# Kernel optimization log

Measured on AMD Instinct MI355X. Metric: run time of the kernel, lower is better.

## Reference

```python
import jax, jax.numpy as jnp
import numpy as np

N, L, H, K, T = 768, 8, 64, 4, 3

def _mlp2(x, w1, b1, w2, b2):
    # Linear -> ReLU -> Linear -> ReLU (matches nn.Sequential in q/k/v MLPs)
    return jax.nn.relu(jax.nn.relu(x @ w1 + b1) @ w2 + b2)

def setup_inputs() -> dict:
    key = jax.random.key(0)
    ks = jax.random.split(key, 20)
    s = 1.0 / np.sqrt(H)
    def lin(k, din, dout):
        return jax.random.uniform(k, (din, dout), jnp.float32, -s, s)
    def bias(k, dout):
        return jax.random.uniform(k, (dout,), jnp.float32, -s, s)
    inp = {
        "h": jax.random.normal(ks[0], (N, L, H), jnp.float32),
        "coord": jax.random.normal(ks[1], (N, L, K, T), jnp.float32),
        "wq1": lin(ks[2], H, H), "bq1": bias(ks[3], H),
        "wq2": lin(ks[4], H, H), "bq2": bias(ks[5], H),
        "wk1": lin(ks[6], H, H), "bk1": bias(ks[7], H),
        "wk2": lin(ks[8], H, H), "bk2": bias(ks[9], H),
        "wv1": lin(ks[10], H, H), "bv1": bias(ks[11], H),
        "wv2": lin(ks[12], H, H), "bv2": bias(ks[13], H),
        "wc1": lin(ks[14], H, H), "bc1": bias(ks[15], H),
        # final coord layer: Linear(H, 4, bias=False), xavier gain=0.001
        "wc2": jax.random.normal(ks[16], (H, K), jnp.float32) * 0.001,
    }
    return inp

def reference(h, coord, wq1, bq1, wq2, bq2, wk1, bk1, wk2, bk2,
              wv1, bv1, wv2, bv2, wc1, bc1, wc2):
    q = _mlp2(h, wq1, bq1, wq2, bq2)          # [N, L, H]
    k = _mlp2(h, wk1, bk1, wk2, bk2)          # [N, L, H]
    v = _mlp2(h, wv1, bv1, wv2, bv2)          # [N, L, H]
    # scores[i, j, l] = <q_i, k_j> per frame l; softmax over neighbor axis j (dim=1)
    scores = jnp.einsum('ilh,jlh->ijl', q, k)
    alpha = jax.nn.softmax(scores, axis=1)     # [N, N, L]
    h_agg = jnp.einsum('ijl,jlh->ilh', alpha, v)
    cmv = jax.nn.relu(v @ wc1 + bc1) @ wc2     # coord_mlp(v): [N, L, 4]
    coord_diff = coord[:, None] - coord[None]  # [N, N, L, 4, 3]
    x_agg = jnp.einsum('ijlkt,ijl,jlk->ilkt', coord_diff, alpha, cmv)
    return (h + h_agg, coord + x_agg)
```

## Files before the change

kernel.cpp:

```cpp
#include <hip/hip_runtime.h>
#include <hip/hip_bf16.h>

#define NN 768
#define LL 8
#define HH 64
#define IT 16
#define SCP 772
#define ABP 776
#define XST 80

typedef __attribute__((ext_vector_type(8))) short bf16x8;
typedef __attribute__((ext_vector_type(4))) float f32x4;

__device__ __forceinline__ short f2bf(float x) {
    union { __hip_bfloat16 h; short s; } u;
    u.h = __float2bfloat16(x);
    return u.s;
}

__device__ __forceinline__ bf16x8 pack8(float4 lo, float4 hi) {
    bf16x8 r;
    r[0] = f2bf(lo.x); r[1] = f2bf(lo.y); r[2] = f2bf(lo.z); r[3] = f2bf(lo.w);
    r[4] = f2bf(hi.x); r[5] = f2bf(hi.y); r[6] = f2bf(hi.z); r[7] = f2bf(hi.w);
    return r;
}

__global__ __launch_bounds__(256) void prep_kernel(
    const float* __restrict__ wq1, const float* __restrict__ wq2,
    const float* __restrict__ wk1, const float* __restrict__ wk2,
    const float* __restrict__ wv1, const float* __restrict__ wv2,
    const float* __restrict__ wc1, const float* __restrict__ wc2,
    short* __restrict__ WT)
{
    const int idx = blockIdx.x * 256 + threadIdx.x;
    if (idx < 28672) {
        const int mm = idx >> 12, rem = idx & 4095;
        const int n = rem >> 6, kk = rem & 63;
        const float* srcs[7] = {wq1, wq2, wk1, wk2, wv1, wv2, wc1};
        WT[idx] = f2bf(srcs[mm][kk * 64 + n]);
    } else if (idx < 29696) {
        const int rem = idx - 28672;
        const int n = rem >> 6, kk = rem & 63;
        WT[idx] = (n < 4) ? f2bf(wc2[kk * 4 + n]) : (short)0;
    }
}

__device__ __forceinline__ void layer_mfma(bf16x8 a0, bf16x8 a1,
                                           const short* __restrict__ WT,
                                           const float* __restrict__ bias,
                                           int m, int quad, bool do_relu,
                                           f32x4 dout[4])
{
    #pragma unroll
    for (int nt = 0; nt < 4; ++nt) {
        const short* wp = WT + (nt * 16 + m) * 64 + quad * 8;
        bf16x8 b0 = *(const bf16x8*)wp;
        bf16x8 b1 = *(const bf16x8*)(wp + 32);
        f32x4 d = {0.f, 0.f, 0.f, 0.f};
        d = __builtin_amdgcn_mfma_f32_16x16x32_bf16(a0, b0, d, 0, 0, 0);
        d = __builtin_amdgcn_mfma_f32_16x16x32_bf16(a1, b1, d, 0, 0, 0);
        if (bias) {
            const float bb = bias[nt * 16 + m];
            #pragma unroll
            for (int rg = 0; rg < 4; ++rg) d[rg] += bb;
        }
        if (do_relu) {
            #pragma unroll
            for (int rg = 0; rg < 4; ++rg) d[rg] = fmaxf(d[rg], 0.f);
        }
        dout[nt] = d;
    }
}

__device__ __forceinline__ void d_to_X(const f32x4 d[4], short (*X)[XST],
                                       int m, int quad) {
    #pragma unroll
    for (int nt = 0; nt < 4; ++nt)
        #pragma unroll
        for (int rg = 0; rg < 4; ++rg)
            X[quad * 4 + rg][nt * 16 + m] = f2bf(d[nt][rg]);
}

__global__ __launch_bounds__(256) void qkv_kernel(
    const float* __restrict__ h, const float* __restrict__ coord,
    const float* __restrict__ bq1, const float* __restrict__ bq2,
    const float* __restrict__ bk1, const float* __restrict__ bk2,
    const float* __restrict__ bv1, const float* __restrict__ bv2,
    const float* __restrict__ bc1,
    const short* __restrict__ WT,
    short* __restrict__ q_ws, short* __restrict__ k_ws,
    short* __restrict__ vT_ws, short* __restrict__ UT_ws)
{
    const int lane = threadIdx.x & 63;
    const int w    = threadIdx.x >> 6;
    const int wid  = blockIdx.x * 4 + w;
    const int chain = wid / 384;
    const int rt    = wid - chain * 384;
    const int r0    = rt * 16;

    const int m    = lane & 15;
    const int quad = lane >> 4;

    __shared__ short Xs[4][16][XST];
    __shared__ float cms[4][16][4];
    short (*X)[XST] = Xs[w];

    const short* WT_q1 = WT;
    const short* WT_q2 = WT + 4096;
    const short* WT_k1 = WT + 8192;
    const short* WT_k2 = WT + 12288;
    const short* WT_v1 = WT + 16384;
    const short* WT_v2 = WT + 20480;
    const short* WT_c1 = WT + 24576;
    const short* WT_c2 = WT + 28672;

    bf16x8 a0, a1;
    {
        const float* hrow = h + (size_t)(r0 + m) * 64;
        a0 = pack8(*(const float4*)(hrow + quad * 8),
                   *(const float4*)(hrow + quad * 8 + 4));
        a1 = pack8(*(const float4*)(hrow + 32 + quad * 8),
                   *(const float4*)(hrow + 32 + quad * 8 + 4));
    }

    f32x4 d[4];

    if (chain == 0) {
        layer_mfma(a0, a1, WT_q1, bq1, m, quad, true, d);
        d_to_X(d, X, m, quad);
        __builtin_amdgcn_wave_barrier();
        a0 = *(const bf16x8*)&X[m][quad * 8];
        a1 = *(const bf16x8*)&X[m][32 + quad * 8];
        layer_mfma(a0, a1, WT_q2, bq2, m, quad, true, d);
        #pragma unroll
        for (int nt = 0; nt < 4; ++nt)
            #pragma unroll
            for (int rg = 0; rg < 4; ++rg) {
                const int g = r0 + quad * 4 + rg, i = g >> 3, l = g & 7;
                q_ws[(l * NN + i) * 64 + nt * 16 + m] = f2bf(d[nt][rg]);
            }
    } else if (chain == 1) {
        layer_mfma(a0, a1, WT_k1, bk1, m, quad, true, d);
        d_to_X(d, X, m, quad);
        __builtin_amdgcn_wave_barrier();
        a0 = *(const bf16x8*)&X[m][quad * 8];
        a1 = *(const bf16x8*)&X[m][32 + quad * 8];
        layer_mfma(a0, a1, WT_k2, bk2, m, quad, true, d);
        #pragma unroll
        for (int nt = 0; nt < 4; ++nt)
            #pragma unroll
            for (int rg = 0; rg < 4; ++rg) {
                const int g = r0 + quad * 4 + rg, i = g >> 3, l = g & 7;
                k_ws[(l * NN + i) * 64 + nt * 16 + m] = f2bf(d[nt][rg]);
            }
    } else {
        layer_mfma(a0, a1, WT_v1, bv1, m, quad, true, d);
        d_to_X(d, X, m, quad);
        __builtin_amdgcn_wave_barrier();
        a0 = *(const bf16x8*)&X[m][quad * 8];
        a1 = *(const bf16x8*)&X[m][32 + quad * 8];
        layer_mfma(a0, a1, WT_v2, bv2, m, quad, true, d);
        #pragma unroll
        for (int nt = 0; nt < 4; ++nt)
            #pragma unroll
            for (int rg = 0; rg < 4; ++rg) {
                const int g = r0 + quad * 4 + rg, i = g >> 3, l = g & 7;
                vT_ws[((size_t)l * 64 + nt * 16 + m) * NN + i] = f2bf(d[nt][rg]);
            }
        d_to_X(d, X, m, quad);
        __builtin_amdgcn_wave_barrier();
        a0 = *(const bf16x8*)&X[m][quad * 8];
        a1 = *(const bf16x8*)&X[m][32 + quad * 8];
        layer_mfma(a0, a1, WT_c1, bc1, m, quad, true, d);
        d_to_X(d, X, m, quad);
        __builtin_amdgcn_wave_barrier();
        a0 = *(const bf16x8*)&X[m][quad * 8];
        a1 = *(const bf16x8*)&X[m][32 + quad * 8];
        {
            const short* wp = WT_c2 + m * 64 + quad * 8;
            bf16x8 b0 = *(const bf16x8*)wp;
            bf16x8 b1 = *(const bf16x8*)(wp + 32);
            f32x4 dc = {0.f, 0.f, 0.f, 0.f};
            dc = __builtin_amdgcn_mfma_f32_16x16x32_bf16(a0, b0, dc, 0, 0, 0);
            dc = __builtin_amdgcn_mfma_f32_16x16x32_bf16(a1, b1, dc, 0, 0, 0);
            if (m < 4) {
                #pragma unroll
                for (int rg = 0; rg < 4; ++rg)
                    cms[w][quad * 4 + rg][m] = dc[rg];
            }
        }
        __builtin_amdgcn_wave_barrier();
        {
            const int row = lane >> 2, kk = lane & 3;
            const float c = cms[w][row][kk];
            const int g = r0 + row, i = g >> 3, l = g & 7;
            UT_ws[((size_t)l * 16 + kk * 4 + 0) * NN + i] = f2bf(c);
            #pragma unroll
            for (int seg = 1; seg < 4; ++seg) {
                const float uval = c * coord[g * 12 + kk * 3 + (seg - 1)];
                UT_ws[((size_t)l * 16 + kk * 4 + seg) * NN + i] = f2bf(uval);
            }
        }
    }
}

__global__ __launch_bounds__(256) void attn_kernel(
    const short* __restrict__ q_ws, const short* __restrict__ k_ws,
    const short* __restrict__ vT_ws, const short* __restrict__ UT_ws,
    const float* __restrict__ h, const float* __restrict__ coord,
    float* __restrict__ h_out, float* __restrict__ x_out)
{
    const int l    = blockIdx.x & 7;
    const int i0   = (blockIdx.x >> 3) * IT;
    const int t    = threadIdx.x;
    const int lane = t & 63;
    const int w    = t >> 6;
    const int m    = lane & 15;
    const int quad = lane >> 4;

    __shared__ float sc[IT][SCP];
    __shared__ alignas(16) short al[IT][ABP];
    __shared__ float rinv_s[IT];
    __shared__ float part3[4][IT][16];
    __shared__ float smS[IT][16];

    const bf16x8 aq0 = *(const bf16x8*)&q_ws[((size_t)l * NN + i0 + m) * 64 + quad * 8];
    const bf16x8 aq1 = *(const bf16x8*)&q_ws[((size_t)l * NN + i0 + m) * 64 + 32 + quad * 8];

    {
        const short* kl = k_ws + (size_t)l * NN * 64;
        for (int nt = 0; nt < 12; ++nt) {
            const int jb = 192 * w + nt * 16;
            const short* krow = kl + (size_t)(jb + m) * 64;
            bf16x8 b0 = *(const bf16x8*)(krow + quad * 8);
            bf16x8 b1 = *(const bf16x8*)(krow + 32 + quad * 8);
            f32x4 d = {0.f, 0.f, 0.f, 0.f};
            d = __builtin_amdgcn_mfma_f32_16x16x32_bf16(aq0, b0, d, 0, 0, 0);
            d = __builtin_amdgcn_mfma_f32_16x16x32_bf16(aq1, b1, d, 0, 0, 0);
            #pragma unroll
            for (int rg = 0; rg < 4; ++rg)
                sc[quad * 4 + rg][jb + m] = d[rg];
        }
    }
    __syncthreads();

    {
        const int r = t >> 4, sub = t & 15;
        float4 v[12];
        #pragma unroll
        for (int jj = 0; jj < 12; ++jj)
            v[jj] = *(const float4*)&sc[r][sub * 4 + 64 * jj];
        float mx = -1e30f;
        #pragma unroll
        for (int jj = 0; jj < 12; ++jj)
            mx = fmaxf(mx, fmaxf(fmaxf(v[jj].x, v[jj].y),
                                 fmaxf(v[jj].z, v[jj].w)));
        mx = fmaxf(mx, __shfl_xor(mx, 1, 64));
        mx = fmaxf(mx, __shfl_xor(mx, 2, 64));
        mx = fmaxf(mx, __shfl_xor(mx, 4, 64));
        mx = fmaxf(mx, __shfl_xor(mx, 8, 64));
        float s = 0.f;
        #pragma unroll
        for (int jj = 0; jj < 12; ++jj) {
            const float e0 = __expf(v[jj].x - mx);
            const float e1 = __expf(v[jj].y - mx);
            const float e2 = __expf(v[jj].z - mx);
            const float e3 = __expf(v[jj].w - mx);
            s += (e0 + e1) + (e2 + e3);
            short4 p;
            p.x = f2bf(e0); p.y = f2bf(e1); p.z = f2bf(e2); p.w = f2bf(e3);
            *(short4*)&al[r][sub * 4 + 64 * jj] = p;
        }
        s += __shfl_xor(s, 1, 64);
        s += __shfl_xor(s, 2, 64);
        s += __shfl_xor(s, 4, 64);
        s += __shfl_xor(s, 8, 64);
        if (sub == 0) rinv_s[r] = 1.f / s;
    }
    __syncthreads();

    {
        f32x4 acc0 = {0.f, 0.f, 0.f, 0.f};
        f32x4 acc1 = {0.f, 0.f, 0.f, 0.f};
        const short* vrow = vT_ws + ((size_t)l * 64 + 16 * w + m) * NN;
        #pragma unroll 4
        for (int kt = 0; kt < 24; kt += 2) {
            const int ka = kt * 32, kb = ka + 32;
            bf16x8 a0 = *(const bf16x8*)&al[m][ka + quad * 8];
            bf16x8 b0 = *(const bf16x8*)(vrow + ka + quad * 8);
            bf16x8 a1 = *(const bf16x8*)&al[m][kb + quad * 8];
            bf16x8 b1 = *(const bf16x8*)(vrow + kb + quad * 8);
            acc0 = __builtin_amdgcn_mfma_f32_16x16x32_bf16(a0, b0, acc0, 0, 0, 0);
            acc1 = __builtin_amdgcn_mfma_f32_16x16x32_bf16(a1, b1, acc1, 0, 0, 0);
        }
        const int c = 16 * w + m;
        #pragma unroll
        for (int rg = 0; rg < 4; ++rg) {
            const int i = quad * 4 + rg;
            const int row = ((i0 + i) * 8 + l) * 64 + c;
            h_out[row] = h[row] + rinv_s[i] * (acc0[rg] + acc1[rg]);
        }
    }

    {
        f32x4 acc = {0.f, 0.f, 0.f, 0.f};
        const short* urow = UT_ws + ((size_t)l * 16 + m) * NN + 192 * w;
        #pragma unroll
        for (int kt = 0; kt < 6; ++kt) {
            const int k0 = kt * 32;
            bf16x8 a = *(const bf16x8*)&al[m][192 * w + k0 + quad * 8];
            bf16x8 b = *(const bf16x8*)(urow + k0 + quad * 8);
            acc = __builtin_amdgcn_mfma_f32_16x16x32_bf16(a, b, acc, 0, 0, 0);
        }
        #pragma unroll
        for (int rg = 0; rg < 4; ++rg)
            part3[w][quad * 4 + rg][m] = acc[rg];
    }
    __syncthreads();
    {
        const int i = t >> 4, u = t & 15;
        smS[i][u] = (part3[0][i][u] + part3[1][i][u] +
                     part3[2][i][u] + part3[3][i][u]) * rinv_s[i];
    }
    __syncthreads();
    if (t < 192) {
        const int i4 = t / 12, kt = t % 12, k4 = kt / 3, s4 = kt % 3;
        const int idx = ((i0 + i4) * 8 + l) * 12 + kt;
        const float cd = coord[idx];
        x_out[idx] = cd + cd * smS[i4][k4 * 4] - smS[i4][k4 * 4 + 1 + s4];
    }
}

extern "C" void kernel_launch(void* const* d_in, const int* in_sizes, int n_in,
                              void* d_out, int out_size, void* d_ws, size_t ws_size,
                              hipStream_t stream) {
    const float* h     = (const float*)d_in[0];
    const float* coord = (const float*)d_in[1];

    float* h_out = (float*)d_out;
    float* x_out = h_out + NN * LL * HH;

    short* q_ws  = (short*)d_ws;
    short* k_ws  = q_ws + NN * LL * HH;
    short* vT_ws = k_ws + NN * LL * HH;
    short* UT_ws = vT_ws + NN * LL * HH;
    short* WT    = UT_ws + NN * LL * 16;

    prep_kernel<<<116, 256, 0, stream>>>(
        (const float*)d_in[2],  (const float*)d_in[4],
        (const float*)d_in[6],  (const float*)d_in[8],
        (const float*)d_in[10], (const float*)d_in[12],
        (const float*)d_in[14], (const float*)d_in[16], WT);

    qkv_kernel<<<288, 256, 0, stream>>>(
        h, coord,
        (const float*)d_in[3],  (const float*)d_in[5],
        (const float*)d_in[7],  (const float*)d_in[9],
        (const float*)d_in[11], (const float*)d_in[13],
        (const float*)d_in[15],
        WT, q_ws, k_ws, vT_ws, UT_ws);

    attn_kernel<<<(NN / IT) * LL, 256, 0, stream>>>(
        q_ws, k_ws, vT_ws, UT_ws, h, coord, h_out, x_out);
}
```

Before: 114.8 us.

## Keep attention scores in registers and compute softmax per wave with cross-wave reduction

Removes the fp32 score tile in shared memory. Each wave now holds its QK^T MFMA results in registers, takes a per-wave row max, reduces it across the four waves through a small LDS array, then exponentiates and writes the bf16 probabilities straight into the alpha tile. This drops a large LDS buffer and its write/read round trip, which can also raise occupancy. In exchange it uses more registers (48 floats of scores per thread), makes scattered 2-byte LDS stores, and recomputes the reciprocal of the sum in each consumer.

```diff
diff --git a/kernel.cpp b/kernel.cpp
--- a/kernel.cpp
+++ b/kernel.cpp
@@ -5,7 +5,6 @@
 #define LL 8
 #define HH 64
 #define IT 16
-#define SCP 772
 #define ABP 776
 #define XST 80
 
@@ -218,17 +217,19 @@
     const int m    = lane & 15;
     const int quad = lane >> 4;
 
-    __shared__ float sc[IT][SCP];
     __shared__ alignas(16) short al[IT][ABP];
-    __shared__ float rinv_s[IT];
+    __shared__ float wmax[4][IT];
+    __shared__ float wsum[4][IT];
     __shared__ float part3[4][IT][16];
     __shared__ float smS[IT][16];
 
     const bf16x8 aq0 = *(const bf16x8*)&q_ws[((size_t)l * NN + i0 + m) * 64 + quad * 8];
     const bf16x8 aq1 = *(const bf16x8*)&q_ws[((size_t)l * NN + i0 + m) * 64 + 32 + quad * 8];
 
+    f32x4 dsc[12];
     {
         const short* kl = k_ws + (size_t)l * NN * 64;
+        #pragma unroll
         for (int nt = 0; nt < 12; ++nt) {
             const int jb = 192 * w + nt * 16;
             const short* krow = kl + (size_t)(jb + m) * 64;
@@ -237,45 +238,49 @@
             f32x4 d = {0.f, 0.f, 0.f, 0.f};
             d = __builtin_amdgcn_mfma_f32_16x16x32_bf16(aq0, b0, d, 0, 0, 0);
             d = __builtin_amdgcn_mfma_f32_16x16x32_bf16(aq1, b1, d, 0, 0, 0);
-            #pragma unroll
-            for (int rg = 0; rg < 4; ++rg)
-                sc[quad * 4 + rg][jb + m] = d[rg];
-        }
+            dsc[nt] = d;
+        }
+    }
+
+    float mx[4];
+    #pragma unroll
+    for (int rg = 0; rg < 4; ++rg) {
+        float mm = dsc[0][rg];
+        #pragma unroll
+        for (int nt = 1; nt < 12; ++nt) mm = fmaxf(mm, dsc[nt][rg]);
+        mm = fmaxf(mm, __shfl_xor(mm, 1, 64));
+        mm = fmaxf(mm, __shfl_xor(mm, 2, 64));
+        mm = fmaxf(mm, __shfl_xor(mm, 4, 64));
+        mm = fmaxf(mm, __shfl_xor(mm, 8, 64));
+        if (m == 0) wmax[w][quad * 4 + rg] = mm;
     }
     __syncthreads();
-
-    {
-        const int r = t >> 4, sub = t & 15;
-        float4 v[12];
-        #pragma unroll
-        for (int jj = 0; jj < 12; ++jj)
-            v[jj] = *(const float4*)&sc[r][sub * 4 + 64 * jj];
-        float mx = -1e30f;
-        #pragma unroll
-        for (int jj = 0; jj < 12; ++jj)
-            mx = fmaxf(mx, fmaxf(fmaxf(v[jj].x, v[jj].y),
-                                 fmaxf(v[jj].z, v[jj].w)));
-        mx = fmaxf(mx, __shfl_xor(mx, 1, 64));
-        mx = fmaxf(mx, __shfl_xor(mx, 2, 64));
-        mx = fmaxf(mx, __shfl_xor(mx, 4, 64));
-        mx = fmaxf(mx, __shfl_xor(mx, 8, 64));
-        float s = 0.f;
-        #pragma unroll
-        for (int jj = 0; jj < 12; ++jj) {
-            const float e0 = __expf(v[jj].x - mx);
-            const float e1 = __expf(v[jj].y - mx);
-            const float e2 = __expf(v[jj].z - mx);
-            const float e3 = __expf(v[jj].w - mx);
-            s += (e0 + e1) + (e2 + e3);
-            short4 p;
-            p.x = f2bf(e0); p.y = f2bf(e1); p.z = f2bf(e2); p.w = f2bf(e3);
-            *(short4*)&al[r][sub * 4 + 64 * jj] = p;
-        }
+    #pragma unroll
+    for (int rg = 0; rg < 4; ++rg) {
+        const int row = quad * 4 + rg;
+        mx[rg] = fmaxf(fmaxf(wmax[0][row], wmax[1][row]),
+                       fmaxf(wmax[2][row], wmax[3][row]));
+    }
+
+    float sl[4] = {0.f, 0.f, 0.f, 0.f};
+    #pragma unroll
+    for (int nt = 0; nt < 12; ++nt) {
+        const int jb = 192 * w + nt * 16;
+        #pragma unroll
+        for (int rg = 0; rg < 4; ++rg) {
+            const float e = __expf(dsc[nt][rg] - mx[rg]);
+            sl[rg] += e;
+            al[quad * 4 + rg][jb + m] = f2bf(e);
+        }
+    }
+    #pragma unroll
+    for (int rg = 0; rg < 4; ++rg) {
+        float s = sl[rg];
         s += __shfl_xor(s, 1, 64);
         s += __shfl_xor(s, 2, 64);
         s += __shfl_xor(s, 4, 64);
         s += __shfl_xor(s, 8, 64);
-        if (sub == 0) rinv_s[r] = 1.f / s;
+        if (m == 0) wsum[w][quad * 4 + rg] = s;
     }
     __syncthreads();
 
@@ -297,8 +302,10 @@
         #pragma unroll
         for (int rg = 0; rg < 4; ++rg) {
             const int i = quad * 4 + rg;
+            const float ri = 1.f / (wsum[0][i] + wsum[1][i] +
+                                    wsum[2][i] + wsum[3][i]);
             const int row = ((i0 + i) * 8 + l) * 64 + c;
-            h_out[row] = h[row] + rinv_s[i] * (acc0[rg] + acc1[rg]);
+            h_out[row] = h[row] + ri * (acc0[rg] + acc1[rg]);
         }
     }
 
@@ -319,8 +326,10 @@
     __syncthreads();
     {
         const int i = t >> 4, u = t & 15;
+        const float ri = 1.f / (wsum[0][i] + wsum[1][i] +
+                                wsum[2][i] + wsum[3][i]);
         smS[i][u] = (part3[0][i][u] + part3[1][i][u] +
-                     part3[2][i][u] + part3[3][i][u]) * rinv_s[i];
+                     part3[2][i][u] + part3[3][i][u]) * ri;
     }
     __syncthreads();
     if (t < 192) {
```

Result: no change. 114.4 us (-0.3%).
